# Optimization experiments

Measured on AMD Instinct MI355X. Metric: run time of the kernel, lower is better.

The kernel has to match this reference:

```python
import math
import jax, jax.numpy as jnp
import numpy as np

ROW, COL = 7, 7          # unfold patch size
KSIZE = 5                # analytic Gaussian kernel size
NUM_POINTS = 100         # logits classes == number of Gaussian prototypes
FEAT_C = 8               # query_rgb uses inp[:, :8] as the splatted feature


def _unfold(x, r, c):
    # nn.Unfold(kernel=(r,c), stride=(r,c)) followed by the reshape in the module
    B, C, H, W = x.shape
    nH, nW = H // r, W // c
    x = x.reshape(B, C, nH, r, nW, c)
    x = jnp.transpose(x, (0, 2, 4, 1, 3, 5))       # [B,nH,nW,C,r,c]
    return x.reshape(B * nH * nW, C, r, c), nH, nW


def _translate_bilinear(img, sx, sy):
    # Equivalent of affine_grid(translation)+grid_sample(align_corners=True, zeros padding)
    # img: [P,H,W]; per-image pixel shifts (sy over rows, sx over cols)
    P, H, W = img.shape
    ii = jnp.broadcast_to(jnp.arange(H, dtype=img.dtype)[None, :, None] + sy[:, None, None], (P, H, W))
    jj = jnp.broadcast_to(jnp.arange(W, dtype=img.dtype)[None, None, :] + sx[:, None, None], (P, H, W))
    i0 = jnp.floor(ii); j0 = jnp.floor(jj)
    wi = ii - i0; wj = jj - j0
    pidx = jnp.arange(P)[:, None, None]

    def gather(iz, jz):
        valid = (iz >= 0) & (iz <= H - 1) & (jz >= 0) & (jz <= W - 1)
        v = img[pidx, jnp.clip(iz, 0, H - 1).astype(jnp.int32), jnp.clip(jz, 0, W - 1).astype(jnp.int32)]
        return jnp.where(valid, v, jnp.zeros((), img.dtype))

    v00 = gather(i0, j0); v01 = gather(i0, j0 + 1.0)
    v10 = gather(i0 + 1.0, j0); v11 = gather(i0 + 1.0, j0 + 1.0)
    return v00 * (1 - wi) * (1 - wj) + v01 * (1 - wi) * wj + v10 * wi * (1 - wj) + v11 * wi * wj


def setup_inputs() -> dict:
    key = jax.random.key(0)
    k1, k2 = jax.random.split(key)
    B, C_IN, H, W = 16, 64, 112, 112
    inp = jax.random.normal(k1, (B, C_IN, H, W), dtype=jnp.float32)
    logits = jax.random.uniform(k2, (B, NUM_POINTS, H, W), dtype=jnp.float32)
    # learned Gaussian prototype parameters (as initialized in __init__)
    lin = jnp.linspace(0.2, 3.0, 10, dtype=jnp.float32)
    sigma_x = jnp.repeat(lin, 10)                # meshgrid 'ij' first output, flattened
    sigma_y = jnp.tile(lin, 10)
    opacity = jax.nn.sigmoid(jnp.ones((NUM_POINTS, 1), jnp.float32))
    rho = jnp.zeros((NUM_POINTS, 1), jnp.float32)
    return {"inp": inp, "logits": logits, "sigma_x": sigma_x, "sigma_y": sigma_y,
            "opacity": opacity, "rho": rho, "scale": 2}


def reference(inp, logits, sigma_x, sigma_y, opacity, rho, scale):
    del scale  # only used for HR sizing in the (truncated) decoder stage
    feat = inp[:, :FEAT_C]
    B, C, H, W = feat.shape
    nH, nW = math.ceil(H / ROW), math.ceil(W / COL)
    up = (nH * ROW, nW * COL)
    if up != (H, W):  # bicubic pre-resize; identity for our H,W (multiples of 7)
        feat = jax.image.resize(feat, (B, C) + up, method='bicubic')
        logits = jax.image.resize(logits, logits.shape[:2] + up, method='bicubic')
    uf, _, _ = _unfold(feat, ROW, COL)           # [BL, C, 7, 7]
    ul, _, _ = _unfold(logits, ROW, COL)         # [BL, K, 7, 7]
    BL = uf.shape[0]
    P = ROW * COL                                # 49 LR points per patch
    # colors at the integer grid coords (fetching_features_from_tensor)
    colors = jnp.transpose(uf.reshape(BL, C, P), (0, 2, 1))   # [BL, P, C]
    # normalized coords: coords_[n] = (col,row); coords_norm = (0.5 - coords/7)*2
    rr, cc = jnp.meshgrid(jnp.arange(ROW, dtype=jnp.float32), jnp.arange(COL, dtype=jnp.float32), indexing='ij')
    tx = 1.0 - 2.0 * cc.reshape(-1) / ROW
    ty = 1.0 - 2.0 * rr.reshape(-1) / COL
    # weighted Gaussian parameters, averaged over the unfolded batch dim
    lbar = jnp.transpose(ul, (0, 2, 3, 1)).reshape(BL, P, NUM_POINTS).mean(axis=0)  # [P,K]
    wsx = lbar @ sigma_x
    wsy = lbar @ sigma_y
    wop = lbar @ opacity[:, 0]
    wrho = lbar @ rho[:, 0]
    # per-point 2x2 covariance and its analytic inverse
    a = wsx ** 2 + 1e-5
    d = wsy ** 2 + 1e-5
    b = wrho * wsx * wsy
    det = a * d - b * b
    ia, ib, idd = d / det, -b / det, a / det
    ax = jnp.linspace(-5.0, 5.0, KSIZE)
    xx = ax[:, None]                             # varies along rows
    yy = ax[None, :]                             # varies along cols
    z = -0.5 * (ia[:, None, None] * xx ** 2 + 2.0 * ib[:, None, None] * xx * yy + idd[:, None, None] * yy ** 2)
    kernel = jnp.exp(z) / (2.0 * jnp.pi * jnp.sqrt(det)[:, None, None])  # [P,5,5]
    kernel = kernel / kernel.max(axis=(-2, -1), keepdims=True)           # peak-normalize
    ph, pw = ROW - KSIZE, COL - KSIZE
    kernel = jnp.pad(kernel, ((0, 0), (ph // 2, ph - ph // 2), (pw // 2, pw - pw // 2)))
    # translate each point's kernel to its location (affine_grid + grid_sample)
    kT = _translate_bilinear(kernel, tx * (COL - 1) / 2.0, ty * (ROW - 1) / 2.0)  # [P,7,7]
    # composite: sum over points of color * opacity * translated kernel
    out_patches = jnp.einsum('bpc,p,pij->bcij', colors, wop, kT)         # [BL,C,7,7]
    # fold patches back into the full feature map
    out = out_patches.reshape(B, nH, nW, C, ROW, COL)
    out = jnp.transpose(out, (0, 3, 1, 4, 2, 5)).reshape(B, C, nH * ROW, nW * COL)
    return out
```

## Files before the change

kernel.cpp:

```cpp
#include <hip/hip_runtime.h>
#include <hip/hip_bf16.h>
#include <math.h>

#define B_      16
#define C_IN    64
#define FEAT_C_ 8
#define H_      112
#define W_      112
#define NH_     16
#define NW_     16
#define NPTS    100
#define P_      49
#define PLANE   (H_*W_)

__global__ void zero_kernel(float* __restrict__ S) {
    int i = blockIdx.x * 256 + threadIdx.x;
    if (i < P_ * NPTS) S[i] = 0.0f;
}

__global__ __launch_bounds__(64) void reduce_kernel(const float* __restrict__ logits,
                                                    float* __restrict__ S) {
    int blk = blockIdx.x;
    int r   = blk % 7;
    int bn  = blk / 7;
    const float* plane = logits + (size_t)bn * PLANE;

    int t = threadIdx.x;
    float acc0 = 0.0f, acc1 = 0.0f;
    #pragma unroll
    for (int k = 0; k < 16; ++k) {
        const float* row = plane + (r + 7 * k) * W_;
        acc0 += row[t];
        if (t < 48) acc1 += row[t + 64];
    }

    __shared__ float bins[7];
    if (t < 7) bins[t] = 0.0f;
    __syncthreads();
    atomicAdd(&bins[t % 7], acc0);
    if (t < 48) atomicAdd(&bins[(t + 64) % 7], acc1);
    __syncthreads();

    if (t < 7) {
        int n = bn % NPTS;
        int p = r * 7 + t;
        atomicAdd(&S[p * NPTS + n], bins[t]);
    }
}

__global__ __launch_bounds__(256) void weights_kernel(const float* __restrict__ S,
                                                      const float* __restrict__ sigx,
                                                      const float* __restrict__ sigy,
                                                      const float* __restrict__ opac,
                                                      const float* __restrict__ rho,
                                                      float* __restrict__ WtT) {
    __shared__ float k7n[P_][P_ + 1];
    __shared__ float wopS[P_];

    int t = threadIdx.x;

    if (t < P_) {
        float wsx = 0.0f, wsy = 0.0f, wop = 0.0f, wrho = 0.0f;
        const float* Sp = S + t * NPTS;
        #pragma unroll
        for (int n = 0; n < NPTS; ++n) {
            float l = Sp[n] * (1.0f / 4096.0f);
            wsx  += l * sigx[n];
            wsy  += l * sigy[n];
            wop  += l * opac[n];
            wrho += l * rho[n];
        }
        wopS[t] = wop;

        float a   = wsx * wsx + 1e-5f;
        float d   = wsy * wsy + 1e-5f;
        float b   = wrho * wsx * wsy;
        float det = a * d - b * b;
        float ia  = d / det, ib = -b / det, idd = a / det;

        float k5[25];
        float kmax = -1e30f;
        #pragma unroll
        for (int i = 0; i < 5; ++i) {
            float x = -5.0f + 2.5f * (float)i;
            #pragma unroll
            for (int j = 0; j < 5; ++j) {
                float y = -5.0f + 2.5f * (float)j;
                float z = -0.5f * (ia * x * x + 2.0f * ib * x * y + idd * y * y);
                float v = expf(z);
                k5[i * 5 + j] = v;
                kmax = fmaxf(kmax, v);
            }
        }
        float inv = 1.0f / kmax;

        #pragma unroll
        for (int q = 0; q < P_; ++q) k7n[t][q] = 0.0f;
        #pragma unroll
        for (int i = 0; i < 5; ++i)
            #pragma unroll
            for (int j = 0; j < 5; ++j)
                k7n[t][(i + 1) * 7 + (j + 1)] = k5[i * 5 + j] * inv;
    }
    __syncthreads();

    for (int idx = t; idx < P_ * P_; idx += 256) {
        int p = idx / P_;
        int q = idx - p * P_;
        int i = q / 7, j = q % 7;
        int r = p / 7, c = p % 7;

        float sx = 3.0f - (6.0f / 7.0f) * (float)c;
        float sy = 3.0f - (6.0f / 7.0f) * (float)r;

        float ii  = (float)i + sy;
        float jj  = (float)j + sx;
        float fi0 = floorf(ii), fj0 = floorf(jj);
        int   i0  = (int)fi0,   j0  = (int)fj0;
        float wi  = ii - fi0,   wj  = jj - fj0;

        bool iv0 = (i0 >= 0)     && (i0 <= 6);
        bool iv1 = (i0 + 1 >= 0) && (i0 + 1 <= 6);
        bool jv0 = (j0 >= 0)     && (j0 <= 6);
        bool jv1 = (j0 + 1 >= 0) && (j0 + 1 <= 6);
        int ci0 = min(max(i0, 0), 6),     cj0 = min(max(j0, 0), 6);
        int ci1 = min(max(i0 + 1, 0), 6), cj1 = min(max(j0 + 1, 0), 6);

        float v00 = (iv0 && jv0) ? k7n[p][ci0 * 7 + cj0] : 0.0f;
        float v01 = (iv0 && jv1) ? k7n[p][ci0 * 7 + cj1] : 0.0f;
        float v10 = (iv1 && jv0) ? k7n[p][ci1 * 7 + cj0] : 0.0f;
        float v11 = (iv1 && jv1) ? k7n[p][ci1 * 7 + cj1] : 0.0f;

        float kt = v00 * (1.0f - wi) * (1.0f - wj)
                 + v01 * (1.0f - wi) * wj
                 + v10 * wi * (1.0f - wj)
                 + v11 * wi * wj;

        WtT[q * P_ + p] = wopS[p] * kt;
    }
}

__global__ __launch_bounds__(64) void apply_kernel(const float* __restrict__ inp,
                                                   const float* __restrict__ WtT,
                                                   float* __restrict__ out) {
    int bl = blockIdx.x * 64 + threadIdx.x;
    int nw = bl & 15;
    int t  = bl >> 4;
    int nh = t & 15;
    t >>= 4;
    int ch    = t & 7;
    int batch = t >> 3;

    const float* src = inp + (((size_t)batch * C_IN    + ch) * H_ + nh * 7) * W_ + nw * 7;
    float*       dst = out + (((size_t)batch * FEAT_C_ + ch) * H_ + nh * 7) * W_ + nw * 7;

    float in[P_];
    #pragma unroll
    for (int r = 0; r < 7; ++r)
        #pragma unroll
        for (int c = 0; c < 7; ++c)
            in[r * 7 + c] = src[r * W_ + c];

    for (int q = 0; q < P_; ++q) {
        const float* w = WtT + q * P_;
        float acc = 0.0f;
        #pragma unroll
        for (int p = 0; p < P_; ++p) acc += in[p] * w[p];
        dst[(q / 7) * W_ + (q % 7)] = acc;
    }
}

extern "C" void kernel_launch(void* const* d_in, const int* in_sizes, int n_in,
                              void* d_out, int out_size, void* d_ws, size_t ws_size,
                              hipStream_t stream) {
    const float* inp    = (const float*)d_in[0];
    const float* logits = (const float*)d_in[1];
    const float* sigx   = (const float*)d_in[2];
    const float* sigy   = (const float*)d_in[3];
    const float* opac   = (const float*)d_in[4];
    const float* rho    = (const float*)d_in[5];

    float* out = (float*)d_out;
    float* S   = (float*)d_ws;
    float* WtT = S + P_ * NPTS;

    zero_kernel<<<(P_ * NPTS + 255) / 256, 256, 0, stream>>>(S);
    reduce_kernel<<<B_ * NPTS * 7, 64, 0, stream>>>(logits, S);
    weights_kernel<<<1, 256, 0, stream>>>(S, sigx, sigy, opac, rho, WtT);
    apply_kernel<<<(B_ * FEAT_C_ * NH_ * NW_) / 64, 64, 0, stream>>>(inp, WtT, out);
}
```

Measured before the change: 195.1 us.

## Fuse weight computation into apply kernel and replace atomics with partial sums

The reduce kernel now sums two batch planes per block and writes per-group partial sums to distinct slots, replacing global atomics and the separate zeroing kernel. The weight-construction logic is merged into the apply kernel: every 448-thread block redundantly reduces the partials, builds the 49x49 weight matrix in shared memory, then each of 7 wavefronts computes one output row of the patch. This removes two launches and the single-block serial weights kernel. The cost is redundant weight computation in every one of 512 blocks and 7x redundant input loads per patch.

Result: faster. 177.0 us (-9.3%).

```diff
diff --git a/kernel.cpp b/kernel.cpp
--- a/kernel.cpp
+++ b/kernel.cpp
@@ -12,26 +12,27 @@
 #define NPTS    100
 #define P_      49
 #define PLANE   (H_*W_)
-
-__global__ void zero_kernel(float* __restrict__ S) {
-    int i = blockIdx.x * 256 + threadIdx.x;
-    if (i < P_ * NPTS) S[i] = 0.0f;
-}
+#define NGRP    8
 
 __global__ __launch_bounds__(64) void reduce_kernel(const float* __restrict__ logits,
-                                                    float* __restrict__ S) {
+                                                    float* __restrict__ Spart) {
     int blk = blockIdx.x;
-    int r   = blk % 7;
-    int bn  = blk / 7;
-    const float* plane = logits + (size_t)bn * PLANE;
+    int g   = blk & 7;
+    int rn  = blk >> 3;
+    int r   = rn % 7;
+    int n   = rn / 7;
+
+    const float* pl0 = logits + ((size_t)(2 * g) * NPTS + n) * PLANE;
+    const float* pl1 = pl0 + (size_t)NPTS * PLANE;
 
     int t = threadIdx.x;
     float acc0 = 0.0f, acc1 = 0.0f;
     #pragma unroll
     for (int k = 0; k < 16; ++k) {
-        const float* row = plane + (r + 7 * k) * W_;
-        acc0 += row[t];
-        if (t < 48) acc1 += row[t + 64];
+        const float* ra = pl0 + (r + 7 * k) * W_;
+        const float* rb = pl1 + (r + 7 * k) * W_;
+        acc0 += ra[t] + rb[t];
+        if (t < 48) acc1 += ra[t + 64] + rb[t + 64];
     }
 
     __shared__ float bins[7];
@@ -42,33 +43,58 @@
     __syncthreads();
 
     if (t < 7) {
-        int n = bn % NPTS;
-        int p = r * 7 + t;
-        atomicAdd(&S[p * NPTS + n], bins[t]);
+        Spart[(r * 7 + t) * (NPTS * NGRP) + n * NGRP + g] = bins[t];
     }
 }
 
-__global__ __launch_bounds__(256) void weights_kernel(const float* __restrict__ S,
-                                                      const float* __restrict__ sigx,
-                                                      const float* __restrict__ sigy,
-                                                      const float* __restrict__ opac,
-                                                      const float* __restrict__ rho,
-                                                      float* __restrict__ WtT) {
+#define NTB 448
+
+__global__ __launch_bounds__(NTB) void fused_kernel(const float* __restrict__ inp,
+                                                    const float* __restrict__ Spart,
+                                                    const float* __restrict__ sigx,
+                                                    const float* __restrict__ sigy,
+                                                    const float* __restrict__ opac,
+                                                    const float* __restrict__ rho,
+                                                    float* __restrict__ out) {
+    __shared__ float ph1[P_][8][4];
     __shared__ float k7n[P_][P_ + 1];
     __shared__ float wopS[P_];
+    __shared__ float WtT[P_ * 52];
 
     int t = threadIdx.x;
+
+    if (t < 392) {
+        int p = t >> 3;
+        int s = t & 7;
+        int n0  = s * 12 + (s < 4 ? s : 4);
+        int len = (s < 4) ? 13 : 12;
+
+        float psx = 0.0f, psy = 0.0f, pop = 0.0f, prh = 0.0f;
+        const float* base = Spart + p * (NPTS * NGRP);
+        for (int e = 0; e < len; ++e) {
+            int n = n0 + e;
+            const float4* sp = (const float4*)(base + n * NGRP);
+            float4 a = sp[0], b = sp[1];
+            float l = (a.x + a.y + a.z + a.w + b.x + b.y + b.z + b.w)
+                      * (1.0f / 4096.0f);
+            psx += l * sigx[n];
+            psy += l * sigy[n];
+            pop += l * opac[n];
+            prh += l * rho[n];
+        }
+        ph1[p][s][0] = psx; ph1[p][s][1] = psy;
+        ph1[p][s][2] = pop; ph1[p][s][3] = prh;
+    }
+    __syncthreads();
 
     if (t < P_) {
         float wsx = 0.0f, wsy = 0.0f, wop = 0.0f, wrho = 0.0f;
-        const float* Sp = S + t * NPTS;
-        #pragma unroll
-        for (int n = 0; n < NPTS; ++n) {
-            float l = Sp[n] * (1.0f / 4096.0f);
-            wsx  += l * sigx[n];
-            wsy  += l * sigy[n];
-            wop  += l * opac[n];
-            wrho += l * rho[n];
+        #pragma unroll
+        for (int s = 0; s < 8; ++s) {
+            wsx  += ph1[t][s][0];
+            wsy  += ph1[t][s][1];
+            wop  += ph1[t][s][2];
+            wrho += ph1[t][s][3];
         }
         wopS[t] = wop;
 
@@ -104,7 +130,7 @@
     }
     __syncthreads();
 
-    for (int idx = t; idx < P_ * P_; idx += 256) {
+    for (int idx = t; idx < P_ * P_; idx += NTB) {
         int p = idx / P_;
         int q = idx - p * P_;
         int i = q / 7, j = q % 7;
@@ -136,20 +162,19 @@
                  + v10 * wi * (1.0f - wj)
                  + v11 * wi * wj;
 
-        WtT[q * P_ + p] = wopS[p] * kt;
-    }
-}
-
-__global__ __launch_bounds__(64) void apply_kernel(const float* __restrict__ inp,
-                                                   const float* __restrict__ WtT,
-                                                   float* __restrict__ out) {
-    int bl = blockIdx.x * 64 + threadIdx.x;
+        WtT[q * 52 + p] = wopS[p] * kt;
+    }
+    __syncthreads();
+
+    int lane = t & 63;
+    int i    = t >> 6;
+    int bl   = blockIdx.x * 64 + lane;
     int nw = bl & 15;
-    int t  = bl >> 4;
-    int nh = t & 15;
-    t >>= 4;
-    int ch    = t & 7;
-    int batch = t >> 3;
+    int u  = bl >> 4;
+    int nh = u & 15;
+    u >>= 4;
+    int ch    = u & 7;
+    int batch = u >> 3;
 
     const float* src = inp + (((size_t)batch * C_IN    + ch) * H_ + nh * 7) * W_ + nw * 7;
     float*       dst = out + (((size_t)batch * FEAT_C_ + ch) * H_ + nh * 7) * W_ + nw * 7;
@@ -161,12 +186,19 @@
         for (int c = 0; c < 7; ++c)
             in[r * 7 + c] = src[r * W_ + c];
 
-    for (int q = 0; q < P_; ++q) {
-        const float* w = WtT + q * P_;
-        float acc = 0.0f;
-        #pragma unroll
-        for (int p = 0; p < P_; ++p) acc += in[p] * w[p];
-        dst[(q / 7) * W_ + (q % 7)] = acc;
+    #pragma unroll
+    for (int j = 0; j < 7; ++j) {
+        const float* w = &WtT[(i * 7 + j) * 52];
+        float a0 = 0.0f, a1 = 0.0f, a2 = 0.0f, a3 = 0.0f;
+        #pragma unroll
+        for (int p4 = 0; p4 < 12; ++p4) {
+            a0 += in[p4 * 4 + 0] * w[p4 * 4 + 0];
+            a1 += in[p4 * 4 + 1] * w[p4 * 4 + 1];
+            a2 += in[p4 * 4 + 2] * w[p4 * 4 + 2];
+            a3 += in[p4 * 4 + 3] * w[p4 * 4 + 3];
+        }
+        float acc = ((a0 + a2) + (a1 + a3)) + in[48] * w[48];
+        dst[i * W_ + j] = acc;
     }
 }
 
@@ -180,12 +212,10 @@
     const float* opac   = (const float*)d_in[4];
     const float* rho    = (const float*)d_in[5];
 
-    float* out = (float*)d_out;
-    float* S   = (float*)d_ws;
-    float* WtT = S + P_ * NPTS;
-
-    zero_kernel<<<(P_ * NPTS + 255) / 256, 256, 0, stream>>>(S);
-    reduce_kernel<<<B_ * NPTS * 7, 64, 0, stream>>>(logits, S);
-    weights_kernel<<<1, 256, 0, stream>>>(S, sigx, sigy, opac, rho, WtT);
-    apply_kernel<<<(B_ * FEAT_C_ * NH_ * NW_) / 64, 64, 0, stream>>>(inp, WtT, out);
+    float* out   = (float*)d_out;
+    float* Spart = (float*)d_ws;
+
+    reduce_kernel<<<NPTS * 7 * NGRP, 64, 0, stream>>>(logits, Spart);
+    fused_kernel<<<(B_ * FEAT_C_ * NH_ * NW_) / 64, NTB, 0, stream>>>(
+        inp, Spart, sigx, sigy, opac, rho, out);
 }
```
